# Performance work log

Measured on AMD Instinct MI355X. Metric: run time of the kernel, lower is better.

## Reference

```python
import jax, jax.numpy as jnp
import numpy as np

D = 96

def setup_inputs() -> dict:
    key = jax.random.key(0)
    ks = jax.random.split(key, 7)
    B, S = 8, 4096
    scale = 1.0 / np.sqrt(D)
    return {
        "h": jax.random.normal(ks[0], (B, S, D), dtype=jnp.float32),
        "Wq": jax.random.normal(ks[1], (D, D), dtype=jnp.float32) * scale,
        "bq": jnp.zeros((D,), dtype=jnp.float32),
        "Wk": jax.random.normal(ks[2], (D, D), dtype=jnp.float32) * scale,
        "bk": jnp.zeros((D,), dtype=jnp.float32),
        "Wv": jax.random.normal(ks[3], (D, D), dtype=jnp.float32) * scale,
        "bv": jnp.zeros((D,), dtype=jnp.float32),
    }

def reference(h, Wq, bq, Wk, bk, Wv, bv):
    # torch Linear: x @ W.T + b
    Q = jnp.einsum('bsd,ed->bse', h, Wq) + bq
    K = jnp.einsum('bsd,ed->bse', h, Wk) + bk
    V = jnp.einsum('bsd,ed->bse', h, Wv) + bv
    scores = jnp.einsum('bse,bte->bst', Q, K) / jnp.sqrt(jnp.float32(D))
    attn = jax.nn.softmax(scores, axis=-1)  # [B,S,S]
    return jnp.einsum('bst,bte->bse', attn, V)
```

## Files before the change

### kernel.cpp

```cpp
#include <hip/hip_runtime.h>

typedef float f32x16 __attribute__((ext_vector_type(16)));
typedef __bf16 bf16x8 __attribute__((ext_vector_type(8)));
typedef const void __attribute__((address_space(1)))* gas_t;
typedef void __attribute__((address_space(3)))* las_t;

__device__ __forceinline__ unsigned short f2bf(float x) {
  union { __bf16 b; unsigned short u; } c; c.b = (__bf16)x; return c.u;
}
__device__ __forceinline__ unsigned pk2(float a, float b) {
  union { __bf16 h[2]; unsigned u; } c;
  c.h[0] = (__bf16)a; c.h[1] = (__bf16)b;
  return c.u;
}
__device__ __forceinline__ float bflo(unsigned u) { return __uint_as_float(u << 16); }
__device__ __forceinline__ float bfhi(unsigned u) { return __uint_as_float(u & 0xffff0000u); }

__global__ __launch_bounds__(256) void qkv_kernel(
    const float* __restrict__ h,
    const float* __restrict__ Wq, const float* __restrict__ bq,
    const float* __restrict__ Wk, const float* __restrict__ bk,
    const float* __restrict__ Wv, const float* __restrict__ bv,
    unsigned short* __restrict__ Qb, unsigned short* __restrict__ Kb,
    unsigned short* __restrict__ Vt)
{
  __shared__ char sm[128*192 + 96*192];
  char* Hsh = sm;
  char* Wsh = sm + 128*192;
  const int tid = threadIdx.x;
  const int blk = blockIdx.x;
  const int w = blockIdx.y;
  const float* W    = (w == 0) ? Wq : (w == 1) ? Wk : Wv;
  const float* bias = (w == 0) ? bq : (w == 1) ? bk : bv;

  #pragma unroll
  for (int i = 0; i < 12; ++i) {
    int idx = tid + 256*i;
    int row = idx / 24, c4 = idx % 24;
    float4 v = *(const float4*)(h + ((size_t)blk*128 + row)*96 + c4*4);
    uint2 pk;
    pk.x = pk2(v.x, v.y);
    pk.y = pk2(v.z, v.w);
    *(uint2*)(Hsh + ((row*192 + c4*8) ^ ((row & 7) << 4))) = pk;
  }
  #pragma unroll
  for (int i = 0; i < 9; ++i) {
    int idx = tid + 256*i;
    int row = idx / 24, c4 = idx % 24;
    float4 v = *(const float4*)(W + row*96 + c4*4);
    uint2 pk;
    pk.x = pk2(v.x, v.y);
    pk.y = pk2(v.z, v.w);
    *(uint2*)(Wsh + ((row*192 + c4*8) ^ ((row & 7) << 4))) = pk;
  }
  __syncthreads();

  const int lane = tid & 63, wv = tid >> 6, hi = lane >> 5, ln = lane & 31;
  const int mrow0 = wv * 32;

  f32x16 acc[3];
  #pragma unroll
  for (int j = 0; j < 3; ++j)
    #pragma unroll
    for (int r = 0; r < 16; ++r) acc[j][r] = 0.f;

  #pragma unroll
  for (int c = 0; c < 6; ++c) {
    bf16x8 af = *(const bf16x8*)(Hsh + (((mrow0 + ln)*192 + c*32 + hi*16) ^ ((ln & 7) << 4)));
    #pragma unroll
    for (int j = 0; j < 3; ++j) {
      bf16x8 bfr = *(const bf16x8*)(Wsh +
                    (((ln + 32*j)*192 + c*32 + hi*16) ^ ((ln & 7) << 4)));
      acc[j] = __builtin_amdgcn_mfma_f32_32x32x16_bf16(af, bfr, acc[j], 0, 0, 0);
    }
  }
  #pragma unroll
  for (int j = 0; j < 3; ++j) {
    const int e = ln + 32*j;
    const float b = bias[e];
    if (w == 2) {
      #pragma unroll
      for (int g = 0; g < 4; ++g) {
        int srow = blk*128 + mrow0 + 8*g + 4*hi;
        int sperm = (srow & ~12) | ((srow & 4) << 1) | ((srow & 8) >> 1);
        int bb = sperm >> 12, s = sperm & 4095;
        uint2 pk;
        pk.x = pk2(acc[j][4*g+0] + b, acc[j][4*g+1] + b);
        pk.y = pk2(acc[j][4*g+2] + b, acc[j][4*g+3] + b);
        *(uint2*)(Vt + ((size_t)bb*96 + e)*4096 + s) = pk;
      }
    } else {
      unsigned short* Outp = (w == 0) ? Qb : Kb;
      const float sc = (w == 0) ? 0.14724443849485857f : 1.0f;
      #pragma unroll
      for (int r = 0; r < 16; ++r) {
        int grow = blk*128 + mrow0 + (r & 3) + 8*(r >> 2) + 4*hi;
        Outp[(size_t)grow*96 + e] = f2bf((acc[j][r] + b) * sc);
      }
    }
  }
}

__global__ __launch_bounds__(128, 2) void flash_kernel(
    const unsigned short* __restrict__ Qb, const unsigned short* __restrict__ Kb,
    const unsigned short* __restrict__ Vt, unsigned short* __restrict__ Opb,
    float* __restrict__ ml, int NT)
{
  __shared__ char sm[2*12288];
  const int tid = threadIdx.x;
  const int lane = tid & 63, wv = tid >> 6, hi = lane >> 5, ln = lane & 31;
  const int qt = blockIdx.x, bb = blockIdx.y, sp = blockIdx.z;
  const int q0 = qt*128 + wv*64;
  const size_t qrowA = (size_t)bb*4096 + q0 + ln;
  const size_t qrowB = qrowA + 32;
  const int sbase = sp * (NT*32);

  const unsigned short* qp = Qb + qrowA*96 + hi*8;

  const unsigned short* Kbase = Kb + ((size_t)bb*4096 + sbase)*96;
  const unsigned short* Vbase = Vt + (size_t)bb*96*4096 + sbase;

  int ksrc[3], vsrc[3], kdb[3];
  #pragma unroll
  for (int i = 0; i < 3; ++i) {
    int d = (tid + 128*i)*16;
    kdb[i] = d;
    int r = d / 192;
    int u = d ^ ((r & 7) << 4);
    if (u / 192 != r) { r = u / 192; u = d ^ ((r & 7) << 4); }
    ksrc[i] = r*96 + ((u - r*192) >> 1);
    int uv = d ^ ((((d >> 6) >> 1) & 7) << 4);
    int e = uv >> 6;
    vsrc[i] = e*4096 + ((uv & 63) >> 1);
  }

  #pragma unroll
  for (int i = 0; i < 3; ++i) {
    __builtin_amdgcn_global_load_lds((gas_t)(const void*)(Kbase + ksrc[i]),
                                     (las_t)(void*)(sm + kdb[i]), 16, 0, 0);
    __builtin_amdgcn_global_load_lds((gas_t)(const void*)(Vbase + vsrc[i]),
                                     (las_t)(void*)(sm + 6144 + kdb[i]), 16, 0, 0);
  }
  __syncthreads();

  f32x16 accA[3], accB[3];
  #pragma unroll
  for (int j = 0; j < 3; ++j)
    #pragma unroll
    for (int r = 0; r < 16; ++r) { accA[j][r] = 0.f; accB[j][r] = 0.f; }

  float lA = 0.f, lB = 0.f;

  for (int st = 0; st < NT; ++st) {
    char* B  = sm + (st & 1)*12288;
    char* Bn = sm + ((st & 1) ^ 1)*12288;

    if (st + 1 < NT) {
      const unsigned short* Kt = Kbase + (st + 1)*32*96;
      const unsigned short* Vp = Vbase + (st + 1)*32;
      #pragma unroll
      for (int i = 0; i < 3; ++i) {
        __builtin_amdgcn_global_load_lds((gas_t)(const void*)(Kt + ksrc[i]),
                                         (las_t)(void*)(Bn + kdb[i]), 16, 0, 0);
        __builtin_amdgcn_global_load_lds((gas_t)(const void*)(Vp + vsrc[i]),
                                         (las_t)(void*)(Bn + 6144 + kdb[i]), 16, 0, 0);
      }
    }

    f32x16 sA, sB;
    #pragma unroll
    for (int r = 0; r < 16; ++r) { sA[r] = 0.f; sB[r] = 0.f; }
    __builtin_amdgcn_s_setprio(1);
    #pragma unroll
    for (int c = 0; c < 6; ++c) {
      bf16x8 k0 = *(const bf16x8*)(B + ((ln*192 + c*32 + hi*16) ^ ((ln & 7) << 4)));
      bf16x8 qa = *(const bf16x8*)(qp + c*16);
      bf16x8 qb = *(const bf16x8*)(qp + 32*96 + c*16);
      sA = __builtin_amdgcn_mfma_f32_32x32x16_bf16(k0, qa, sA, 0, 0, 0);
      sB = __builtin_amdgcn_mfma_f32_32x32x16_bf16(k0, qb, sB, 0, 0, 0);
    }
    __builtin_amdgcn_s_setprio(0);

    #pragma unroll
    for (int r = 0; r < 16; ++r) { sA[r] = __builtin_amdgcn_exp2f(sA[r]); }
    #pragma unroll
    for (int r = 0; r < 16; ++r) { sB[r] = __builtin_amdgcn_exp2f(sB[r]); }
    {
      float t0 = 0.f, t1 = 0.f, u0 = 0.f, u1 = 0.f;
      #pragma unroll
      for (int r = 0; r < 8; ++r) {
        t0 += sA[r]; t1 += sA[r + 8];
        u0 += sB[r]; u1 += sB[r + 8];
      }
      lA += t0 + t1;
      lB += u0 + u1;
    }

    bf16x8 pfA[2], pfB[2];
    #pragma unroll
    for (int c1 = 0; c1 < 2; ++c1) {
      union { bf16x8 v; unsigned u[4]; } fa, fb;
      #pragma unroll
      for (int k = 0; k < 4; ++k) {
        fa.u[k] = pk2(sA[c1*8 + 2*k], sA[c1*8 + 2*k + 1]);
        fb.u[k] = pk2(sB[c1*8 + 2*k], sB[c1*8 + 2*k + 1]);
      }
      pfA[c1] = fa.v; pfB[c1] = fb.v;
    }

    __builtin_amdgcn_s_setprio(1);
    #pragma unroll
    for (int c1 = 0; c1 < 2; ++c1) {
      #pragma unroll
      for (int j = 0; j < 3; ++j) {
        const int e = ln + 32*j;
        bf16x8 vf = *(const bf16x8*)(B + 6144 +
                      ((e*64 + c1*32 + hi*16) ^ (((e >> 1) & 7) << 4)));
        accA[j] = __builtin_amdgcn_mfma_f32_32x32x16_bf16(vf, pfA[c1], accA[j], 0, 0, 0);
        accB[j] = __builtin_amdgcn_mfma_f32_32x32x16_bf16(vf, pfB[c1], accB[j], 0, 0, 0);
      }
    }
    __builtin_amdgcn_s_setprio(0);

    __syncthreads();
  }

  lA += __shfl_xor(lA, 32, 64);
  lB += __shfl_xor(lB, 32, 64);
  unsigned short* OrowA = Opb + ((size_t)sp*3145728 + qrowA*96);
  unsigned short* OrowB = Opb + ((size_t)sp*3145728 + qrowB*96);
  #pragma unroll
  for (int j = 0; j < 3; ++j)
    #pragma unroll
    for (int g = 0; g < 4; ++g) {
      uint2 oa, ob;
      oa.x = pk2(accA[j][4*g+0], accA[j][4*g+1]);
      oa.y = pk2(accA[j][4*g+2], accA[j][4*g+3]);
      ob.x = pk2(accB[j][4*g+0], accB[j][4*g+1]);
      ob.y = pk2(accB[j][4*g+2], accB[j][4*g+3]);
      *(uint2*)(OrowA + 32*j + 8*g + 4*hi) = oa;
      *(uint2*)(OrowB + 32*j + 8*g + 4*hi) = ob;
    }
  if (hi == 0) {
    ml[(size_t)sp*32768 + qrowA] = lA;
    ml[(size_t)sp*32768 + qrowB] = lB;
  }
}

__global__ __launch_bounds__(256) void combine_kernel(
    const unsigned short* __restrict__ Opb, const float* __restrict__ ml,
    float* __restrict__ out)
{
  const int g = blockIdx.x*256 + threadIdx.x;
  const int row = g / 12, e8 = (g % 12) * 8;
  float ls = 0.f;
  #pragma unroll
  for (int s = 0; s < 4; ++s) ls += ml[(size_t)s*32768 + row];
  const float inv = 1.0f / ls;
  float acc[8] = {0.f, 0.f, 0.f, 0.f, 0.f, 0.f, 0.f, 0.f};
  #pragma unroll
  for (int s = 0; s < 4; ++s) {
    uint4 d = *(const uint4*)(Opb + (size_t)s*3145728 + (size_t)row*96 + e8);
    acc[0] += bflo(d.x); acc[1] += bfhi(d.x);
    acc[2] += bflo(d.y); acc[3] += bfhi(d.y);
    acc[4] += bflo(d.z); acc[5] += bfhi(d.z);
    acc[6] += bflo(d.w); acc[7] += bfhi(d.w);
  }
  float4 o0 = make_float4(acc[0]*inv, acc[1]*inv, acc[2]*inv, acc[3]*inv);
  float4 o1 = make_float4(acc[4]*inv, acc[5]*inv, acc[6]*inv, acc[7]*inv);
  float* po = out + (size_t)row*96 + e8;
  *(float4*)(po) = o0;
  *(float4*)(po + 4) = o1;
}

extern "C" void kernel_launch(void* const* d_in, const int* in_sizes, int n_in,
                              void* d_out, int out_size, void* d_ws, size_t ws_size,
                              hipStream_t stream) {
  const float* h  = (const float*)d_in[0];
  const float* Wq = (const float*)d_in[1];
  const float* bq = (const float*)d_in[2];
  const float* Wk = (const float*)d_in[3];
  const float* bk = (const float*)d_in[4];
  const float* Wv = (const float*)d_in[5];
  const float* bv = (const float*)d_in[6];
  float* out = (float*)d_out;
  char* ws = (char*)d_ws;
  unsigned short* Qb  = (unsigned short*)(ws);
  unsigned short* Kb  = (unsigned short*)(ws + 6291456);
  unsigned short* Vt  = (unsigned short*)(ws + 12582912);
  unsigned short* Opb = (unsigned short*)(ws + 18874368);
  float*          mlp = (float*)(ws + 44040192);

  qkv_kernel<<<dim3(256, 3), 256, 0, stream>>>(h, Wq, bq, Wk, bk, Wv, bv, Qb, Kb, Vt);
  flash_kernel<<<dim3(32, 8, 4), 128, 0, stream>>>(Qb, Kb, Vt, Opb, mlp, 32);
  combine_kernel<<<1536, 256, 0, stream>>>(Opb, mlp, out);
}
```

Baseline: 82.07 us.

## Triple-buffer K/V tiles with vmcnt waits and hoist Q fragments into registers

```diff
diff --git a/kernel.cpp b/kernel.cpp
--- a/kernel.cpp
+++ b/kernel.cpp
@@ -106,7 +106,7 @@
     const unsigned short* __restrict__ Vt, unsigned short* __restrict__ Opb,
     float* __restrict__ ml, int NT)
 {
-  __shared__ char sm[2*12288];
+  __shared__ char sm[3*12288];
   const int tid = threadIdx.x;
   const int lane = tid & 63, wv = tid >> 6, hi = lane >> 5, ln = lane & 31;
   const int qt = blockIdx.x, bb = blockIdx.y, sp = blockIdx.z;
@@ -115,7 +115,15 @@
   const size_t qrowB = qrowA + 32;
   const int sbase = sp * (NT*32);
 
-  const unsigned short* qp = Qb + qrowA*96 + hi*8;
+  bf16x8 qa[6], qb[6];
+  {
+    const unsigned short* qp = Qb + qrowA*96 + hi*8;
+    #pragma unroll
+    for (int c = 0; c < 6; ++c) {
+      qa[c] = *(const bf16x8*)(qp + c*16);
+      qb[c] = *(const bf16x8*)(qp + 32*96 + c*16);
+    }
+  }
 
   const unsigned short* Kbase = Kb + ((size_t)bb*4096 + sbase)*96;
   const unsigned short* Vbase = Vt + (size_t)bb*96*4096 + sbase;
@@ -141,7 +149,13 @@
     __builtin_amdgcn_global_load_lds((gas_t)(const void*)(Vbase + vsrc[i]),
                                      (las_t)(void*)(sm + 6144 + kdb[i]), 16, 0, 0);
   }
-  __syncthreads();
+  #pragma unroll
+  for (int i = 0; i < 3; ++i) {
+    __builtin_amdgcn_global_load_lds((gas_t)(const void*)(Kbase + 3072 + ksrc[i]),
+                                     (las_t)(void*)(sm + 12288 + kdb[i]), 16, 0, 0);
+    __builtin_amdgcn_global_load_lds((gas_t)(const void*)(Vbase + 32 + vsrc[i]),
+                                     (las_t)(void*)(sm + 12288 + 6144 + kdb[i]), 16, 0, 0);
+  }
 
   f32x16 accA[3], accB[3];
   #pragma unroll
@@ -152,12 +166,20 @@
   float lA = 0.f, lB = 0.f;
 
   for (int st = 0; st < NT; ++st) {
-    char* B  = sm + (st & 1)*12288;
-    char* Bn = sm + ((st & 1) ^ 1)*12288;
-
-    if (st + 1 < NT) {
-      const unsigned short* Kt = Kbase + (st + 1)*32*96;
-      const unsigned short* Vp = Vbase + (st + 1)*32;
+    if (st < NT - 1) {
+      asm volatile("s_waitcnt vmcnt(6)" ::: "memory");
+    } else {
+      asm volatile("s_waitcnt vmcnt(0)" ::: "memory");
+    }
+    __builtin_amdgcn_s_barrier();
+    asm volatile("" ::: "memory");
+
+    char* B = sm + (st % 3)*12288;
+
+    if (st + 2 < NT) {
+      char* Bn = sm + ((st + 2) % 3)*12288;
+      const unsigned short* Kt = Kbase + (st + 2)*3072;
+      const unsigned short* Vp = Vbase + (st + 2)*32;
       #pragma unroll
       for (int i = 0; i < 3; ++i) {
         __builtin_amdgcn_global_load_lds((gas_t)(const void*)(Kt + ksrc[i]),
@@ -174,10 +196,8 @@
     #pragma unroll
     for (int c = 0; c < 6; ++c) {
       bf16x8 k0 = *(const bf16x8*)(B + ((ln*192 + c*32 + hi*16) ^ ((ln & 7) << 4)));
-      bf16x8 qa = *(const bf16x8*)(qp + c*16);
-      bf16x8 qb = *(const bf16x8*)(qp + 32*96 + c*16);
-      sA = __builtin_amdgcn_mfma_f32_32x32x16_bf16(k0, qa, sA, 0, 0, 0);
-      sB = __builtin_amdgcn_mfma_f32_32x32x16_bf16(k0, qb, sB, 0, 0, 0);
+      sA = __builtin_amdgcn_mfma_f32_32x32x16_bf16(k0, qa[c], sA, 0, 0, 0);
+      sB = __builtin_amdgcn_mfma_f32_32x32x16_bf16(k0, qb[c], sB, 0, 0, 0);
     }
     __builtin_amdgcn_s_setprio(0);
 
@@ -221,8 +241,6 @@
       }
     }
     __builtin_amdgcn_s_setprio(0);
-
-    __syncthreads();
   }
 
   lA += __shfl_xor(lA, 32, 64);
```

Measured after the change: 83.14 us. No clear change (+1.3%).
